# Performance work log

Hardware: AMD Instinct MI355X
Metric: run time of the kernel (lower is better)

The kernel has to match this reference:

```python
import jax, jax.numpy as jnp
import numpy as np

B, S, D = 128, 50, 128
NUM_NODE = 40000
SAMPLE = 12
HOP = 2
ALPHA = 0.2  # leaky-relu slope (opt.alpha)


def _leaky(x, slope=ALPHA):
    return jnp.where(x >= 0, x, slope * x)


def setup_inputs() -> dict:
    key = jax.random.key(0)
    ks = jax.random.split(key, 12)
    stdv = 1.0 / float(np.sqrt(D))
    inputs = jax.random.randint(ks[0], (B, S), 0, NUM_NODE)
    adj = jax.random.randint(ks[1], (B, S, S), 0, 5)
    mask_item = jax.random.randint(ks[2], (B, S), 0, 2).at[:, 0].set(1)
    item = jax.random.randint(ks[3], (B, S), 0, NUM_NODE)
    adj_all = jax.random.randint(ks[4], (NUM_NODE, SAMPLE), 0, NUM_NODE)
    num_weight = jax.random.uniform(ks[5], (NUM_NODE, SAMPLE), dtype=jnp.float32)
    embedding = jax.random.uniform(ks[6], (NUM_NODE, D), minval=-stdv, maxval=stdv, dtype=jnp.float32)
    a_local = jax.random.uniform(ks[7], (4, D), minval=-stdv, maxval=stdv, dtype=jnp.float32)
    agg_w1 = jax.random.uniform(ks[8], (HOP, D + 1, D), minval=-stdv, maxval=stdv, dtype=jnp.float32)
    agg_w2 = jax.random.uniform(ks[9], (HOP, D, 1), minval=-stdv, maxval=stdv, dtype=jnp.float32)
    agg_w3 = jax.random.uniform(ks[10], (HOP, 2 * D, D), minval=-stdv, maxval=stdv, dtype=jnp.float32)
    return dict(inputs=inputs, adj=adj, mask_item=mask_item, item=item,
                adj_all=adj_all, num_weight=num_weight, embedding=embedding,
                a_local=a_local, agg_w1=agg_w1, agg_w2=agg_w2, agg_w3=agg_w3)


def _local_agg(h, adj, a_local):
    # e_k[b,i,j] = leakyrelu(sum_d h[b,i,d]*h[b,j,d]*a_k[d]); never materialize [B,N,N,D]
    e = _leaky(jnp.einsum('bid,bjd,kd->kbij', h, h, a_local))  # [4,B,S,S]
    alpha = jnp.full(e.shape[1:], -9e15, dtype=h.dtype)
    for k in range(4):
        alpha = jnp.where(adj == k + 1, e[k], alpha)
    alpha = jax.nn.softmax(alpha, axis=-1)
    return alpha @ h


def _global_agg(w1, w2, w3, self_v, neigh_v, neigh_w, extra):
    # self_v [B,L,D]; neigh_v [B,L,SAMPLE,D]; neigh_w [B,L,SAMPLE]; extra [B,L,D]
    feat = jnp.concatenate([extra[:, :, None, :] * neigh_v, neigh_w[..., None]], axis=-1)  # [B,L,SAMPLE,D+1]
    a = _leaky(feat @ w1, 0.2)                              # [B,L,SAMPLE,D]
    a = jax.nn.softmax((a @ w2)[..., 0], axis=-1)[..., None]  # [B,L,SAMPLE,1]
    neigh = jnp.sum(a * neigh_v, axis=-2)                   # [B,L,D]
    out = jnp.concatenate([self_v, neigh], axis=-1) @ w3    # [B,L,D]
    return jax.nn.relu(out)


def _forward(inputs, adj, mask_item, item, adj_all, num_weight, embedding,
             a_local, agg_w1, agg_w2, agg_w3):
    h = embedding[inputs]                          # [B,S,D]
    h_local = _local_agg(h, adj, a_local)
    # multi-hop neighbor sampling (index_select into adj_all / num)
    item_neighbors = [inputs]
    weight_neighbors = []
    support = S
    for _ in range(HOP):
        last = item_neighbors[-1].reshape(-1)
        support *= SAMPLE
        item_neighbors.append(adj_all[last].reshape(B, support))
        weight_neighbors.append(num_weight[last].reshape(B, support))
    entity = [embedding[idx] for idx in item_neighbors]
    mask_f = mask_item.astype(h.dtype)
    item_emb = embedding[item] * mask_f[..., None]
    session = (jnp.sum(item_emb, 1) / jnp.sum(mask_f, -1, keepdims=True))[:, None, :]  # [B,1,D]
    for n_hop in range(HOP):
        nxt = []
        for hop in range(HOP - n_hop):
            self_v = entity[hop]
            L = self_v.shape[1]
            neigh_v = entity[hop + 1].reshape(B, L, SAMPLE, D)
            neigh_w = weight_neighbors[hop].reshape(B, L, SAMPLE)
            extra = jnp.broadcast_to(session, (B, L, D))
            nxt.append(_global_agg(agg_w1[n_hop], agg_w2[n_hop], agg_w3[n_hop],
                                   self_v, neigh_v, neigh_w, extra))
        entity = nxt
    h_global = entity[0].reshape(B, S, D)
    # dropout_local / dropout_global are identity in eval mode
    return h_local + h_global


def reference(inputs, adj, mask_item, item, adj_all, num_weight, embedding,
              a_local, agg_w1, agg_w2, agg_w3):
    return _forward(inputs, adj, mask_item, item, adj_all, num_weight, embedding,
                    a_local, agg_w1, agg_w2, agg_w3)
```

## Files before the change

### kernel.cpp

```cpp
#include <hip/hip_runtime.h>
#include <math.h>

#define BATCH 128
#define S 50
#define D 128
#define SAMPLE 12

typedef __attribute__((ext_vector_type(8))) short short8v;
typedef __attribute__((ext_vector_type(4))) float f32x4;
typedef unsigned short u16;

__device__ __forceinline__ float leakyf(float x) { return x >= 0.f ? x : 0.2f * x; }
__device__ __forceinline__ u16 f2bf(float f) {
    union { float f; unsigned u; } v; v.f = f;
    unsigned u = v.u;
    return (u16)((u + 0x7FFFu + ((u >> 16) & 1u)) >> 16);
}
__device__ __forceinline__ float bf2f(u16 h) {
    union { float f; unsigned u; } v; v.u = ((unsigned)h) << 16; return v.f;
}

__global__ __launch_bounds__(256) void setup1_kernel(
    const int* __restrict__ item, const int* __restrict__ mask,
    const int* __restrict__ inputs, const int* __restrict__ adj_all,
    const float* __restrict__ num_weight, const float* __restrict__ emb,
    float* __restrict__ session, int* __restrict__ n1, float* __restrict__ nw0)
{
    const int bx = blockIdx.x, t = threadIdx.x;
    if (bx < BATCH) {
        if (t < 128) {
            float num = 0.f, den = 0.f;
            for (int s = 0; s < S; ++s) {
                float m = (float)mask[bx * S + s];
                num += m * emb[item[bx * S + s] * D + t];
                den += m;
            }
            session[bx * D + t] = num / den;
        }
    } else {
        int idx = (bx - BATCH) * 256 + t;
        if (idx < BATCH * 600) {
            int b = idx / 600, j = idx % 600;
            int node = inputs[b * S + j / SAMPLE];
            n1[idx]  = adj_all[node * SAMPLE + j % SAMPLE];
            nw0[idx] = num_weight[node * SAMPLE + j % SAMPLE];
        }
    }
}

__global__ __launch_bounds__(256) void prep2_kernel(
    const float* __restrict__ emb, const float* __restrict__ w1,
    const float* __restrict__ w3, const float* __restrict__ session,
    const int* __restrict__ adj_all, const float* __restrict__ num_weight,
    const int* __restrict__ n1,
    u16* __restrict__ emb_bf, u16* __restrict__ sw1, u16* __restrict__ w3t,
    int* __restrict__ n2p, int* __restrict__ n1p, float* __restrict__ nw1)
{
    const int bx = blockIdx.x, t = threadIdx.x;
    if (bx < 2500) {
        int idx = bx * 256 + t;
        const float4* src = reinterpret_cast<const float4*>(emb) + (size_t)idx * 2;
        float4 a = src[0], c = src[1];
        u16 o[8] = {f2bf(a.x), f2bf(a.y), f2bf(a.z), f2bf(a.w),
                    f2bf(c.x), f2bf(c.y), f2bf(c.z), f2bf(c.w)};
        *reinterpret_cast<uint4*>(emb_bf + (size_t)idx * 8) = *reinterpret_cast<uint4*>(o);
    } else if (bx < 2756) {
        int id = bx - 2500, hop = id >> 7, b = id & 127;
        const float* w1s = w1 + hop * 129 * 128;
        const float* se = session + b * 128;
        int n = t >> 1, kh = (t & 1) * 64;
        u16* dst = sw1 + (((size_t)(hop * 128 + b) * 128 + n) * 128) + kh;
        for (int kq = 0; kq < 64; kq += 8) {
            u16 o[8];
            #pragma unroll
            for (int e = 0; e < 8; ++e) { int k = kh + kq + e; o[e] = f2bf(w1s[k * 128 + n] * se[k]); }
            *reinterpret_cast<uint4*>(dst + kq) = *reinterpret_cast<uint4*>(o);
        }
    } else if (bx < 2788) {
        int j = (bx - 2756) * 256 + t;
        int hop = j >> 12, r = j & 4095, n = r >> 5, k0 = (r & 31) * 8;
        const float* w3s = w3 + hop * 256 * 128;
        u16 o[8];
        #pragma unroll
        for (int e = 0; e < 8; ++e) o[e] = f2bf(w3s[(k0 + e) * 128 + n]);
        *reinterpret_cast<uint4*>(w3t + ((size_t)hop * 128 + n) * 256 + k0) = *reinterpret_cast<uint4*>(o);
    } else if (bx < 6388) {
        int idx = (bx - 2788) * 256 + t;
        if (idx < BATCH * 7200) {
            int b = idx / 7200, r = idx % 7200;
            int lblk = r / 96, q = r % 96;
            int i = q >> 4, c = q & 15;
            int gm = lblk * 96 + (c >> 2) * 24 + i * 4 + (c & 3);
            int node = n1[b * 600 + gm / SAMPLE];
            int s = gm % SAMPLE;
            n2p[idx] = adj_all[node * SAMPLE + s] << 8;
            nw1[b * 7200 + gm] = num_weight[node * SAMPLE + s];
        }
    } else {
        int idx = (bx - 6388) * 256 + t;
        if (idx < BATCH * 672) {
            int b = idx / 672, r = idx % 672;
            int lblk = r / 96, q = r % 96;
            int i = q >> 4, c = q & 15;
            int gm = lblk * 96 + (c >> 2) * 24 + i * 4 + (c & 3);
            int jc = (gm < 600) ? gm : 0;
            n1p[idx] = n1[b * 600 + jc] << 8;
        }
    }
}

__device__ __forceinline__ int swz(int cg, int kk) { return ((kk & 1) << 2) | cg; }

template <int PATH>
__global__ __launch_bounds__(256, 4) void main_kernel(
    const int* __restrict__ inputs, const int* __restrict__ adj,
    const u16* __restrict__ emb_bf, const float* __restrict__ a_local,
    const int* __restrict__ n1, const int* __restrict__ n2p,
    const int* __restrict__ n1p,
    const float* __restrict__ nw0, const float* __restrict__ nw1,
    const u16* __restrict__ sw1, const float* __restrict__ w1,
    const float* __restrict__ w2, const u16* __restrict__ w3t,
    const u16* __restrict__ in0, const u16* __restrict__ in1,
    u16* __restrict__ o0, u16* __restrict__ o1, float* __restrict__ outf)
{
    __shared__ __align__(16) char smem[35072];
    const int b = blockIdx.y;
    const int t = threadIdx.x;
    const int bx = blockIdx.x;

    if (PATH == 0 && bx == 0) {
        u16*   ht    = (u16*)smem;
        float* alpha = (float*)(smem + 13312);
        u16*   alb   = (u16*)(smem + 23520);

        for (int idx = t; idx < S * D; idx += 256) {
            int i = idx >> 7, d = idx & 127;
            ht[d * 52 + i] = emb_bf[(size_t)inputs[b * S + i] * D + d];
        }
        for (int idx = t; idx < 512; idx += 256) alb[idx] = f2bf(a_local[idx]);
        __syncthreads();

        for (int p = t; p < S * S; p += 256) {
            int i = p / S, j = p % S;
            int a = adj[b * S * S + p];
            float v = -9e15f;
            if (a >= 1 && a <= 4) {
                const u16* ak = alb + (a - 1) * D;
                float dot = 0.f;
                #pragma unroll 4
                for (int d = 0; d < D; ++d)
                    dot += bf2f(ht[d * 52 + i]) * bf2f(ht[d * 52 + j]) * bf2f(ak[d]);
                v = leakyf(dot);
            }
            alpha[i * 51 + j] = v;
        }
        __syncthreads();

        if (t < S) {
            float m = -INFINITY;
            for (int j = 0; j < S; ++j) m = fmaxf(m, alpha[t * 51 + j]);
            float ssum = 0.f;
            for (int j = 0; j < S; ++j) { float e = __expf(alpha[t * 51 + j] - m); alpha[t * 51 + j] = e; ssum += e; }
            float inv = 1.f / ssum;
            for (int j = 0; j < S; ++j) alpha[t * 51 + j] *= inv;
        }
        __syncthreads();

        for (int idx = t; idx < S * D; idx += 256) {
            int i = idx >> 7, d = idx & 127;
            float acc = 0.f;
            #pragma unroll 5
            for (int j = 0; j < S; ++j) acc += alpha[i * 51 + j] * bf2f(ht[d * 52 + j]);
            outf[(size_t)b * S * D + idx] = acc;
        }
        return;
    }

    int mode, lblk, L, Lm, hop;
    const u16 *nsrc, *ssrc;
    const int* ptab; const float* nwTab;
    u16* outb;
    if (PATH == 2)    { mode = 2; lblk = bx;     L = 50;  Lm = 600;  hop = 1; nsrc = in1;    ssrc = in0;    ptab = nullptr;                   nwTab = nw0; outb = nullptr; }
    else if (bx >= 8) { mode = 1; lblk = bx - 8; L = 600; Lm = 7200; hop = 0; nsrc = emb_bf; ssrc = emb_bf; ptab = n2p + (b * 75 + lblk) * 96; nwTab = nw1; outb = o1; }
    else              { mode = 0; lblk = bx - 1; L = 50;  Lm = 600;  hop = 0; nsrc = emb_bf; ssrc = emb_bf; ptab = n1p + (b * 7 + lblk) * 96;  nwTab = nw0; outb = o0; }
    const int l0 = lblk * 8;

    u16*   nvL     = (u16*)smem;
    u16*   A2      = (u16*)(smem + 24576);
    float* score_w = (float*)(smem + 32768);
    float* nwgtL   = (float*)(smem + 34304);
    float* alphL   = (float*)(smem + 34688);

    const u16*   sw1b   = sw1 + (size_t)(hop * 128 + b) * 16384;
    const float* w1last = w1 + hop * 129 * 128 + 128 * 128;
    const float* w2h    = w2 + hop * 128;
    const u16*   w3th   = w3t + hop * 32768;

    const int lane = t & 63, wv = t >> 6, cn = lane & 15, cg = lane >> 4;
    const int nc0 = (2 * wv) * 16 + cn, nc1 = (2 * wv + 1) * 16 + cn;
    const int cS = t & 15;
    const int chunk = t >> 4;

    {
        int kkS = t >> 6, cgS = (t >> 4) & 3;
        int cn2 = cS ^ swz(cgS, kkS);
        #pragma unroll
        for (int i = 0; i < 6; ++i) {
            int off;
            if (PATH == 2) {
                int gm = l0 * 12 + (cn2 >> 2) * 24 + i * 4 + (cn2 & 3);
                if (gm > 599) gm = 599;
                off = (b * 600 + gm) << 8;
            } else {
                off = ptab[i * 16 + cn2];
            }
            uint4 v = *reinterpret_cast<const uint4*>((const char*)nsrc + (unsigned)off + chunk * 16);
            *reinterpret_cast<uint4*>(nvL + (i * 256 + t) * 8) = v;
        }
    }
    {
        uint4 v = make_uint4(0, 0, 0, 0);
        if (cS < 8) {
            int lg = l0 + cS; if (lg >= L) lg = 0;
            int srow;
            if (PATH == 2)      srow = b * 50 + lg;
            else if (mode == 1) srow = n1[b * 600 + lg];
            else                srow = inputs[b * S + lg];
            v = *reinterpret_cast<const uint4*>(ssrc + (size_t)srow * 128 + chunk * 8);
        }
        *reinterpret_cast<uint4*>(A2 + t * 8) = v;
    }
    if (t < 128) {
        int slot = (4 + (t >> 5)) * 64 + ((t >> 3) & 3) * 16 + 8 + (t & 7);
        *reinterpret_cast<uint4*>(A2 + slot * 8) = make_uint4(0, 0, 0, 0);
    }
    if (t < 96) {
        int gm = l0 * 12 + t;
        nwgtL[t] = (gm < Lm) ? nwTab[b * Lm + gm] : 0.f;
    }
    __syncthreads();

    f32x4 acc[6][2];
    #pragma unroll
    for (int mt = 0; mt < 6; ++mt) {
        acc[mt][0] = (f32x4){0.f, 0.f, 0.f, 0.f};
        acc[mt][1] = (f32x4){0.f, 0.f, 0.f, 0.f};
    }
    #pragma unroll
    for (int kk = 0; kk < 4; ++kk) {
        int kb = kk * 32 + cg * 8;
        int lslot = cg * 16 + (cn ^ swz(cg, kk));
        short8v b0 = *reinterpret_cast<const short8v*>(sw1b + nc0 * 128 + kb);
        short8v b1 = *reinterpret_cast<const short8v*>(sw1b + nc1 * 128 + kb);
        #pragma unroll
        for (int mt = 0; mt < 6; ++mt) {
            short8v a = *reinterpret_cast<const short8v*>(nvL + ((mt * 4 + kk) * 64 + lslot) * 8);
            acc[mt][0] = __builtin_amdgcn_mfma_f32_16x16x32_bf16(a, b0, acc[mt][0], 0, 0, 0);
            acc[mt][1] = __builtin_amdgcn_mfma_f32_16x16x32_bf16(a, b1, acc[mt][1], 0, 0, 0);
        }
    }
    {
        float w2v0 = w2h[nc0], w2v1 = w2h[nc1];
        float w1l0 = w1last[nc0], w1l1 = w1last[nc1];
        #pragma unroll
        for (int mt = 0; mt < 6; ++mt) {
            #pragma unroll
            for (int r = 0; r < 4; ++r) {
                int m = cg * 24 + mt * 4 + r;
                float nw = nwgtL[m];
                float v = leakyf(acc[mt][0][r] + nw * w1l0) * w2v0 +
                          leakyf(acc[mt][1][r] + nw * w1l1) * w2v1;
                v += __shfl_xor(v, 1); v += __shfl_xor(v, 2);
                v += __shfl_xor(v, 4); v += __shfl_xor(v, 8);
                if (cn == 0) score_w[m * 4 + wv] = v;
            }
        }
    }
    __syncthreads();

    {
        float alph[24];
        const f32x4* sw4 = reinterpret_cast<const f32x4*>(score_w);
        float mx0 = -1e30f, mx1 = -1e30f;
        #pragma unroll
        for (int q = 0; q < 24; ++q) {
            f32x4 s4 = sw4[cg * 24 + q];
            float s = (s4[0] + s4[1]) + (s4[2] + s4[3]);
            alph[q] = s;
            if (q < 12) mx0 = fmaxf(mx0, s); else mx1 = fmaxf(mx1, s);
        }
        float sm0 = 0.f, sm1 = 0.f;
        #pragma unroll
        for (int q = 0; q < 12; ++q) { alph[q] = __expf(alph[q] - mx0); sm0 += alph[q]; }
        #pragma unroll
        for (int q = 12; q < 24; ++q) { alph[q] = __expf(alph[q] - mx1); sm1 += alph[q]; }
        float i0 = 1.f / sm0, i1 = 1.f / sm1;
        if (cn == 0) {
            #pragma unroll
            for (int q = 0; q < 12; ++q)  alphL[(cg * 2) * 12 + q] = alph[q] * i0;
            #pragma unroll
            for (int q = 12; q < 24; ++q) alphL[(cg * 2 + 1) * 12 + (q - 12)] = alph[q] * i1;
        }
    }

    #pragma unroll 1
    for (int i = 0; i < 4; ++i) {
        int idx = i * 256 + t;
        int l = idx >> 7, d = idx & 127;
        int kkd = d >> 5, cgd = (d >> 3) & 3, el = d & 7;
        int cnb = (l >> 1) * 4;
        int mtb = (l & 1) * 3;
        int fd = swz(cgd, kkd);
        float a = 0.f;
        #pragma unroll
        for (int s = 0; s < 12; ++s) {
            int slot = ((mtb + (s >> 2)) * 4 + kkd) * 64 + cgd * 16 + ((cnb + (s & 3)) ^ fd);
            a += alphL[l * 12 + s] * bf2f(nvL[slot * 8 + el]);
        }
        int slot2 = (4 + kkd) * 64 + cgd * 16 + l;
        A2[slot2 * 8 + el] = f2bf(a);
    }
    __syncthreads();

    #pragma unroll
    for (int j = 0; j < 2; ++j) {
        int nc = (2 * wv + j) * 16 + cn;
        f32x4 acc2 = (f32x4){0.f, 0.f, 0.f, 0.f};
        #pragma unroll
        for (int kk2 = 0; kk2 < 8; ++kk2) {
            short8v a2 = *reinterpret_cast<const short8v*>(A2 + (kk2 * 64 + lane) * 8);
            short8v bb = *reinterpret_cast<const short8v*>(w3th + nc * 256 + kk2 * 32 + cg * 8);
            acc2 = __builtin_amdgcn_mfma_f32_16x16x32_bf16(a2, bb, acc2, 0, 0, 0);
        }
        if (cg < 2) {
            #pragma unroll
            for (int r = 0; r < 4; ++r) {
                int l = cg * 4 + r;
                int lg = l0 + l;
                float v = fmaxf(acc2[r], 0.f);
                if (lg < L) {
                    if (PATH == 2) { float* p = outf + ((size_t)b * 50 + lg) * 128 + nc; *p += v; }
                    else           outb[((size_t)b * L + lg) * 128 + nc] = f2bf(v);
                }
            }
        }
    }
}

extern "C" void kernel_launch(void* const* d_in, const int* in_sizes, int n_in,
                              void* d_out, int out_size, void* d_ws, size_t ws_size,
                              hipStream_t stream)
{
    const int*   inputs     = (const int*)d_in[0];
    const int*   adj        = (const int*)d_in[1];
    const int*   mask_item  = (const int*)d_in[2];
    const int*   item       = (const int*)d_in[3];
    const int*   adj_all    = (const int*)d_in[4];
    const float* num_weight = (const float*)d_in[5];
    const float* embedding  = (const float*)d_in[6];
    const float* a_local    = (const float*)d_in[7];
    const float* agg_w1     = (const float*)d_in[8];
    const float* agg_w2     = (const float*)d_in[9];
    const float* agg_w3     = (const float*)d_in[10];
    float* out = (float*)d_out;

    char* w = (char*)d_ws;
    float* ws_session = (float*)(w);
    int*   ws_n1      = (int*)(w + 65536);
    float* ws_nw0     = (float*)(w + 372736);
    float* ws_nw1     = (float*)(w + 679936);
    int*   ws_n2p     = (int*)(w + 4366336);
    int*   ws_n1p     = (int*)(w + 8052736);
    u16*   ws_emb     = (u16*)(w + 8396800);
    u16*   ws_sw1     = (u16*)(w + 18636800);
    u16*   ws_w3t     = (u16*)(w + 27025408);
    u16*   ws_out0    = (u16*)(w + 27156480);
    u16*   ws_out1    = (u16*)(w + 28794880);

    setup1_kernel<<<dim3(BATCH + 300), 256, 0, stream>>>(
        item, mask_item, inputs, adj_all, num_weight, embedding,
        ws_session, ws_n1, ws_nw0);
    prep2_kernel<<<dim3(6724), 256, 0, stream>>>(
        embedding, agg_w1, agg_w3, ws_session, adj_all, num_weight, ws_n1,
        ws_emb, ws_sw1, ws_w3t, ws_n2p, ws_n1p, ws_nw1);

    main_kernel<0><<<dim3(83, BATCH), 256, 0, stream>>>(
        inputs, adj, ws_emb, a_local, ws_n1, ws_n2p, ws_n1p, ws_nw0, ws_nw1,
        ws_sw1, agg_w1, agg_w2, ws_w3t,
        nullptr, nullptr, ws_out0, ws_out1, out);

    main_kernel<2><<<dim3(7, BATCH), 256, 0, stream>>>(
        inputs, adj, ws_emb, a_local, ws_n1, ws_n2p, ws_n1p, ws_nw0, ws_nw1,
        ws_sw1, agg_w1, agg_w2, ws_w3t,
        ws_out0, ws_out1, nullptr, nullptr, out);
}
```

Baseline: 356.6 us.

## Double main kernel block size so each wave owns one 16-column MFMA tile

The main kernel moves from 256 to 512 threads per block, so each of eight waves computes a single 16-column output tile instead of two. The score reduction, softmax and weighted neighbour sum are reworked to match: the softmax now uses wave shuffles per row, and the alpha-weighted sum is split across all waves using packed bf16 pair loads. The aim is more waves in flight and fewer registers per thread to hide gather and LDS latency. The cost is a larger LDS footprint, more partial scores to combine, and a tighter launch-bounds occupancy target.

```diff
diff --git a/kernel.cpp b/kernel.cpp
--- a/kernel.cpp
+++ b/kernel.cpp
@@ -19,6 +19,7 @@
 __device__ __forceinline__ float bf2f(u16 h) {
     union { float f; unsigned u; } v; v.u = ((unsigned)h) << 16; return v.f;
 }
+__device__ __forceinline__ int swz(int cg, int kk) { return ((kk & 1) << 2) | cg; }
 
 __global__ __launch_bounds__(256) void setup1_kernel(
     const int* __restrict__ item, const int* __restrict__ mask,
@@ -109,10 +110,8 @@
     }
 }
 
-__device__ __forceinline__ int swz(int cg, int kk) { return ((kk & 1) << 2) | cg; }
-
 template <int PATH>
-__global__ __launch_bounds__(256, 4) void main_kernel(
+__global__ __launch_bounds__(512, 6) void main_kernel(
     const int* __restrict__ inputs, const int* __restrict__ adj,
     const u16* __restrict__ emb_bf, const float* __restrict__ a_local,
     const int* __restrict__ n1, const int* __restrict__ n2p,
@@ -123,7 +122,7 @@
     const u16* __restrict__ in0, const u16* __restrict__ in1,
     u16* __restrict__ o0, u16* __restrict__ o1, float* __restrict__ outf)
 {
-    __shared__ __align__(16) char smem[35072];
+    __shared__ __align__(16) char smem[36736];
     const int b = blockIdx.y;
     const int t = threadIdx.x;
     const int bx = blockIdx.x;
@@ -133,14 +132,14 @@
         float* alpha = (float*)(smem + 13312);
         u16*   alb   = (u16*)(smem + 23520);
 
-        for (int idx = t; idx < S * D; idx += 256) {
+        for (int idx = t; idx < S * D; idx += 512) {
             int i = idx >> 7, d = idx & 127;
             ht[d * 52 + i] = emb_bf[(size_t)inputs[b * S + i] * D + d];
         }
-        for (int idx = t; idx < 512; idx += 256) alb[idx] = f2bf(a_local[idx]);
+        if (t < 512) alb[t] = f2bf(a_local[t]);
         __syncthreads();
 
-        for (int p = t; p < S * S; p += 256) {
+        for (int p = t; p < S * S; p += 512) {
             int i = p / S, j = p % S;
             int a = adj[b * S * S + p];
             float v = -9e15f;
@@ -166,7 +165,7 @@
         }
         __syncthreads();
 
-        for (int idx = t; idx < S * D; idx += 256) {
+        for (int idx = t; idx < S * D; idx += 512) {
             int i = idx >> 7, d = idx & 127;
             float acc = 0.f;
             #pragma unroll 5
@@ -180,7 +179,7 @@
     const u16 *nsrc, *ssrc;
     const int* ptab; const float* nwTab;
     u16* outb;
-    if (PATH == 2)    { mode = 2; lblk = bx;     L = 50;  Lm = 600;  hop = 1; nsrc = in1;    ssrc = in0;    ptab = nullptr;                   nwTab = nw0; outb = nullptr; }
+    if (PATH == 2)    { mode = 2; lblk = bx;     L = 50;  Lm = 600;  hop = 1; nsrc = in1;    ssrc = in0;    ptab = nullptr;                    nwTab = nw0; outb = nullptr; }
     else if (bx >= 8) { mode = 1; lblk = bx - 8; L = 600; Lm = 7200; hop = 0; nsrc = emb_bf; ssrc = emb_bf; ptab = n2p + (b * 75 + lblk) * 96; nwTab = nw1; outb = o1; }
     else              { mode = 0; lblk = bx - 1; L = 50;  Lm = 600;  hop = 0; nsrc = emb_bf; ssrc = emb_bf; ptab = n1p + (b * 7 + lblk) * 96;  nwTab = nw0; outb = o0; }
     const int l0 = lblk * 8;
@@ -188,8 +187,8 @@
     u16*   nvL     = (u16*)smem;
     u16*   A2      = (u16*)(smem + 24576);
     float* score_w = (float*)(smem + 32768);
-    float* nwgtL   = (float*)(smem + 34304);
-    float* alphL   = (float*)(smem + 34688);
+    float* nwgtL   = (float*)(smem + 35840);
+    float* alphw   = (float*)(smem + 36224);
 
     const u16*   sw1b   = sw1 + (size_t)(hop * 128 + b) * 16384;
     const float* w1last = w1 + hop * 129 * 128 + 128 * 128;
@@ -197,28 +196,27 @@
     const u16*   w3th   = w3t + hop * 32768;
 
     const int lane = t & 63, wv = t >> 6, cn = lane & 15, cg = lane >> 4;
-    const int nc0 = (2 * wv) * 16 + cn, nc1 = (2 * wv + 1) * 16 + cn;
-    const int cS = t & 15;
-    const int chunk = t >> 4;
-
-    {
-        int kkS = t >> 6, cgS = (t >> 4) & 3;
+    const int nc = wv * 16 + cn;
+
+    #pragma unroll
+    for (int i = 0; i < 3; ++i) {
+        int slot = i * 512 + t;
+        int mt = slot >> 8, kkS = (slot >> 6) & 3;
+        int cgS = (slot >> 4) & 3, cS = slot & 15;
         int cn2 = cS ^ swz(cgS, kkS);
-        #pragma unroll
-        for (int i = 0; i < 6; ++i) {
-            int off;
-            if (PATH == 2) {
-                int gm = l0 * 12 + (cn2 >> 2) * 24 + i * 4 + (cn2 & 3);
-                if (gm > 599) gm = 599;
-                off = (b * 600 + gm) << 8;
-            } else {
-                off = ptab[i * 16 + cn2];
-            }
-            uint4 v = *reinterpret_cast<const uint4*>((const char*)nsrc + (unsigned)off + chunk * 16);
-            *reinterpret_cast<uint4*>(nvL + (i * 256 + t) * 8) = v;
-        }
-    }
-    {
+        unsigned off;
+        if (PATH == 2) {
+            int gm = l0 * 12 + (cn2 >> 2) * 24 + mt * 4 + (cn2 & 3);
+            if (gm > 599) gm = 599;
+            off = (unsigned)((b * 600 + gm) << 8);
+        } else {
+            off = (unsigned)ptab[mt * 16 + cn2];
+        }
+        uint4 v = *reinterpret_cast<const uint4*>((const char*)nsrc + off + (kkS * 4 + cgS) * 16);
+        *reinterpret_cast<uint4*>(nvL + slot * 8) = v;
+    }
+    if (t < 256) {
+        int chunk = t >> 4, cS = t & 15;
         uint4 v = make_uint4(0, 0, 0, 0);
         if (cS < 8) {
             int lg = l0 + cS; if (lg >= L) lg = 0;
@@ -229,102 +227,89 @@
             v = *reinterpret_cast<const uint4*>(ssrc + (size_t)srow * 128 + chunk * 8);
         }
         *reinterpret_cast<uint4*>(A2 + t * 8) = v;
-    }
-    if (t < 128) {
-        int slot = (4 + (t >> 5)) * 64 + ((t >> 3) & 3) * 16 + 8 + (t & 7);
+    } else if (t < 384) {
+        int t2 = t & 127;
+        int slot = (4 + (t2 >> 5)) * 64 + ((t2 >> 3) & 3) * 16 + 8 + (t2 & 7);
         *reinterpret_cast<uint4*>(A2 + slot * 8) = make_uint4(0, 0, 0, 0);
-    }
-    if (t < 96) {
-        int gm = l0 * 12 + t;
-        nwgtL[t] = (gm < Lm) ? nwTab[b * Lm + gm] : 0.f;
+    } else if (t < 480) {
+        int m = t - 384;
+        int gm = l0 * 12 + m;
+        nwgtL[m] = (gm < Lm) ? nwTab[b * Lm + gm] : 0.f;
     }
     __syncthreads();
 
-    f32x4 acc[6][2];
+    f32x4 acc[6];
     #pragma unroll
-    for (int mt = 0; mt < 6; ++mt) {
-        acc[mt][0] = (f32x4){0.f, 0.f, 0.f, 0.f};
-        acc[mt][1] = (f32x4){0.f, 0.f, 0.f, 0.f};
-    }
+    for (int mt = 0; mt < 6; ++mt) acc[mt] = (f32x4){0.f, 0.f, 0.f, 0.f};
     #pragma unroll
     for (int kk = 0; kk < 4; ++kk) {
-        int kb = kk * 32 + cg * 8;
+        short8v bF = *reinterpret_cast<const short8v*>(sw1b + nc * 128 + kk * 32 + cg * 8);
         int lslot = cg * 16 + (cn ^ swz(cg, kk));
-        short8v b0 = *reinterpret_cast<const short8v*>(sw1b + nc0 * 128 + kb);
-        short8v b1 = *reinterpret_cast<const short8v*>(sw1b + nc1 * 128 + kb);
         #pragma unroll
         for (int mt = 0; mt < 6; ++mt) {
             short8v a = *reinterpret_cast<const short8v*>(nvL + ((mt * 4 + kk) * 64 + lslot) * 8);
-            acc[mt][0] = __builtin_amdgcn_mfma_f32_16x16x32_bf16(a, b0, acc[mt][0], 0, 0, 0);
-            acc[mt][1] = __builtin_amdgcn_mfma_f32_16x16x32_bf16(a, b1, acc[mt][1], 0, 0, 0);
+            acc[mt] = __builtin_amdgcn_mfma_f32_16x16x32_bf16(a, bF, acc[mt], 0, 0, 0);
         }
     }
     {
-        float w2v0 = w2h[nc0], w2v1 = w2h[nc1];
-        float w1l0 = w1last[nc0], w1l1 = w1last[nc1];
+        float w2v = w2h[nc], w1lv = w1last[nc];
         #pragma unroll
         for (int mt = 0; mt < 6; ++mt) {
             #pragma unroll
             for (int r = 0; r < 4; ++r) {
                 int m = cg * 24 + mt * 4 + r;
-                float nw = nwgtL[m];
-                float v = leakyf(acc[mt][0][r] + nw * w1l0) * w2v0 +
-                          leakyf(acc[mt][1][r] + nw * w1l1) * w2v1;
+                float v = leakyf(acc[mt][r] + nwgtL[m] * w1lv) * w2v;
                 v += __shfl_xor(v, 1); v += __shfl_xor(v, 2);
                 v += __shfl_xor(v, 4); v += __shfl_xor(v, 8);
-                if (cn == 0) score_w[m * 4 + wv] = v;
+                if (cn == 0) score_w[m * 8 + wv] = v;
             }
         }
     }
     __syncthreads();
 
     {
-        float alph[24];
-        const f32x4* sw4 = reinterpret_cast<const f32x4*>(score_w);
-        float mx0 = -1e30f, mx1 = -1e30f;
-        #pragma unroll
-        for (int q = 0; q < 24; ++q) {
-            f32x4 s4 = sw4[cg * 24 + q];
-            float s = (s4[0] + s4[1]) + (s4[2] + s4[3]);
-            alph[q] = s;
-            if (q < 12) mx0 = fmaxf(mx0, s); else mx1 = fmaxf(mx1, s);
-        }
-        float sm0 = 0.f, sm1 = 0.f;
-        #pragma unroll
-        for (int q = 0; q < 12; ++q) { alph[q] = __expf(alph[q] - mx0); sm0 += alph[q]; }
-        #pragma unroll
-        for (int q = 12; q < 24; ++q) { alph[q] = __expf(alph[q] - mx1); sm1 += alph[q]; }
-        float i0 = 1.f / sm0, i1 = 1.f / sm1;
-        if (cn == 0) {
-            #pragma unroll
-            for (int q = 0; q < 12; ++q)  alphL[(cg * 2) * 12 + q] = alph[q] * i0;
-            #pragma unroll
-            for (int q = 12; q < 24; ++q) alphL[(cg * 2 + 1) * 12 + (q - 12)] = alph[q] * i1;
-        }
-    }
-
-    #pragma unroll 1
-    for (int i = 0; i < 4; ++i) {
-        int idx = i * 256 + t;
-        int l = idx >> 7, d = idx & 127;
-        int kkd = d >> 5, cgd = (d >> 3) & 3, el = d & 7;
-        int cnb = (l >> 1) * 4;
-        int mtb = (l & 1) * 3;
-        int fd = swz(cgd, kkd);
-        float a = 0.f;
-        #pragma unroll
-        for (int s = 0; s < 12; ++s) {
-            int slot = ((mtb + (s >> 2)) * 4 + kkd) * 64 + cgd * 16 + ((cnb + (s & 3)) ^ fd);
-            a += alphL[l * 12 + s] * bf2f(nvL[slot * 8 + el]);
-        }
-        int slot2 = (4 + kkd) * 64 + cgd * 16 + l;
-        A2[slot2 * 8 + el] = f2bf(a);
+        float sval = -1e30f;
+        if (cn < 12) {
+            int m = wv * 12 + cn;
+            f32x4 p0 = *reinterpret_cast<const f32x4*>(score_w + m * 8);
+            f32x4 p1 = *reinterpret_cast<const f32x4*>(score_w + m * 8 + 4);
+            sval = ((p0[0] + p0[1]) + (p0[2] + p0[3])) +
+                   ((p1[0] + p1[1]) + (p1[2] + p1[3]));
+        }
+        float mx = sval;
+        mx = fmaxf(mx, __shfl_xor(mx, 1)); mx = fmaxf(mx, __shfl_xor(mx, 2));
+        mx = fmaxf(mx, __shfl_xor(mx, 4)); mx = fmaxf(mx, __shfl_xor(mx, 8));
+        float e = (cn < 12) ? __expf(sval - mx) : 0.f;
+        float sm = e;
+        sm += __shfl_xor(sm, 1); sm += __shfl_xor(sm, 2);
+        sm += __shfl_xor(sm, 4); sm += __shfl_xor(sm, 8);
+        if (cn < 12 && cg == 0) alphw[wv * 16 + cn] = e / sm;
+    }
+
+    {
+        const int q = wv >> 1;
+        const int remB = (wv & 1) * 12;
+        const int d2 = lane;
+        const int kk = d2 >> 4, cg2 = (d2 >> 2) & 3;
+        const int fd = swz(cg2, kk);
+        float a0 = 0.f, a1 = 0.f;
+        #pragma unroll
+        for (int s2 = 0; s2 < 12; ++s2) {
+            int rem = remB + s2;
+            int slot = ((rem >> 2) * 4 + kk) * 64 + cg2 * 16 + (((q << 2) | (rem & 3)) ^ fd);
+            unsigned pk = *reinterpret_cast<const unsigned*>(
+                (const char*)nvL + slot * 16 + (d2 & 3) * 4);
+            float al = alphw[wv * 16 + s2];
+            a0 += al * bf2f((u16)(pk & 0xffff));
+            a1 += al * bf2f((u16)(pk >> 16));
+        }
+        unsigned pk2 = ((unsigned)f2bf(a1) << 16) | f2bf(a0);
+        int slot2 = (4 + (d2 >> 4)) * 64 + cg2 * 16 + wv;
+        *reinterpret_cast<unsigned*>((char*)A2 + slot2 * 16 + (d2 & 3) * 4) = pk2;
     }
     __syncthreads();
 
-    #pragma unroll
-    for (int j = 0; j < 2; ++j) {
-        int nc = (2 * wv + j) * 16 + cn;
+    {
         f32x4 acc2 = (f32x4){0.f, 0.f, 0.f, 0.f};
         #pragma unroll
         for (int kk2 = 0; kk2 < 8; ++kk2) {
@@ -335,8 +320,7 @@
         if (cg < 2) {
             #pragma unroll
             for (int r = 0; r < 4; ++r) {
-                int l = cg * 4 + r;
-                int lg = l0 + l;
+                int lg = l0 + cg * 4 + r;
                 float v = fmaxf(acc2[r], 0.f);
                 if (lg < L) {
                     if (PATH == 2) { float* p = outf + ((size_t)b * 50 + lg) * 128 + nc; *p += v; }
@@ -384,12 +368,12 @@
         embedding, agg_w1, agg_w3, ws_session, adj_all, num_weight, ws_n1,
         ws_emb, ws_sw1, ws_w3t, ws_n2p, ws_n1p, ws_nw1);
 
-    main_kernel<0><<<dim3(83, BATCH), 256, 0, stream>>>(
+    main_kernel<0><<<dim3(83, BATCH), 512, 0, stream>>>(
         inputs, adj, ws_emb, a_local, ws_n1, ws_n2p, ws_n1p, ws_nw0, ws_nw1,
         ws_sw1, agg_w1, agg_w2, ws_w3t,
         nullptr, nullptr, ws_out0, ws_out1, out);
 
-    main_kernel<2><<<dim3(7, BATCH), 256, 0, stream>>>(
+    main_kernel<2><<<dim3(7, BATCH), 512, 0, stream>>>(
         inputs, adj, ws_emb, a_local, ws_n1, ws_n2p, ws_n1p, ws_nw0, ws_nw1,
         ws_sw1, agg_w1, agg_w2, ws_w3t,
         ws_out0, ws_out1, nullptr, nullptr, out);
```

New measurement: 369.1 us. 3.5% more time.
